# Performance work log

Hardware: AMD Instinct MI355X
Metric: run time of the kernel (lower is better)

Reference implementation:

```python
import jax, jax.numpy as jnp
import numpy as np

N, H, E, G, OUT = 50000, 128, 600000, 256, 64
NUM_ITERS = 5
GAMMA = 0.1
EPS = 0.1
NEG_SLOPE = 0.01


def setup_inputs() -> dict:
    key = jax.random.key(0)
    ks = jax.random.split(key, 10)
    s = 1.0 / np.sqrt(H)
    x = jax.random.normal(ks[0], (N, H), dtype=jnp.float32)
    edge_index = jax.random.randint(ks[1], (2, E), 0, N, dtype=jnp.int64)
    batch = jnp.sort(jax.random.randint(ks[2], (N,), 0, G, dtype=jnp.int64))
    W = jax.random.normal(ks[3], (H, H), dtype=jnp.float32) * s
    bias = jax.random.normal(ks[4], (H,), dtype=jnp.float32) * s
    lin_w = jax.random.normal(ks[5], (H, H), dtype=jnp.float32) * s
    l1_w = jax.random.normal(ks[6], (3 * H // 2, 3 * H), dtype=jnp.float32) / np.sqrt(3 * H)
    l1_b = jax.random.normal(ks[7], (3 * H // 2,), dtype=jnp.float32) * 0.01
    l2_w = jax.random.normal(ks[8], (OUT, 3 * H // 2), dtype=jnp.float32) / np.sqrt(3 * H // 2)
    l2_b = jax.random.normal(ks[9], (OUT,), dtype=jnp.float32) * 0.01
    return {"x": x, "edge_index": edge_index, "batch": batch, "W": W, "bias": bias,
            "lin_w": lin_w, "l1_w": l1_w, "l1_b": l1_b, "l2_w": l2_w, "l2_b": l2_b}


def reference(x, edge_index, batch, W, bias, lin_w, l1_w, l1_b, l2_w, l2_b):
    n = x.shape[0]
    src, dst = edge_index[0], edge_index[1]
    # antisymmetric weight: W - W^T - gamma*I
    A = W - W.T - GAMMA * jnp.eye(W.shape[0], dtype=x.dtype)
    for _ in range(NUM_ITERS):
        neigh = x @ lin_w.T                                   # [N,H] linear (no bias)
        agg = jax.ops.segment_sum(neigh[src], dst, num_segments=n)  # gather-scatter add
        conv = x @ A.T + agg + bias
        x = x + EPS * jnp.tanh(conv)
    # triple global pooling per graph: add / max / mean
    add = jax.ops.segment_sum(x, batch, num_segments=G)
    mx = jax.ops.segment_max(x, batch, num_segments=G)
    cnt = jax.ops.segment_sum(jnp.ones((n,), dtype=x.dtype), batch, num_segments=G)
    safe_cnt = jnp.maximum(cnt, 1.0)[:, None]
    mean = add / safe_cnt
    mx = jnp.where(cnt[:, None] > 0, mx, 0.0)
    pooled = jnp.concatenate([add, mx, mean], axis=1)          # [G, 3H]
    h = jax.nn.leaky_relu(pooled @ l1_w.T + l1_b, NEG_SLOPE)
    out = jax.nn.leaky_relu(h @ l2_w.T + l2_b, NEG_SLOPE)
    return out
```

## Files before the change

### kernel.cpp

```cpp
#include <hip/hip_runtime.h>
#include <hip/hip_fp16.h>
#include <cmath>

#define H 128
#define GAMMA 0.1f
#define EPS 0.1f
#define NEG 0.01f
#define NGRAPH 256

typedef _Float16 half_t;
typedef _Float16 f16x8 __attribute__((ext_vector_type(8)));
typedef _Float16 f16x4 __attribute__((ext_vector_type(4)));
typedef _Float16 f16x2 __attribute__((ext_vector_type(2)));
typedef float f32x4 __attribute__((ext_vector_type(4)));

__device__ __forceinline__ float fast_tanh(float v) {
    float e = __builtin_amdgcn_exp2f(v * 2.8853900817779268f);
    float r = __builtin_amdgcn_rcpf(e + 1.0f);
    return 1.0f - 2.0f * r;
}

__global__ void prep_kernel(const float* __restrict__ W, const float* __restrict__ lin_w,
                            half_t* __restrict__ WtT) {
    int idx = blockIdx.x * 256 + threadIdx.x;
    int j = idx >> 8, k = idx & 255;
    float v;
    if (k < H) v = W[j * H + k] - W[k * H + j] - (j == k ? GAMMA : 0.f);
    else       v = lin_w[j * H + (k - H)];
    WtT[j * 256 + k] = (half_t)v;
}

__global__ void cast_kernel(const float* __restrict__ x, half_t* __restrict__ xh, int n4) {
    int i = blockIdx.x * 256 + threadIdx.x;
    if (i < n4) {
        float4 v = *(const float4*)(x + (size_t)i * 4);
        half_t* o = xh + (size_t)i * 4;
        o[0] = (half_t)v.x; o[1] = (half_t)v.y; o[2] = (half_t)v.z; o[3] = (half_t)v.w;
    }
}

__global__ void count_kernel(const int* __restrict__ dst, int* __restrict__ deg, int E) {
    int e = blockIdx.x * blockDim.x + threadIdx.x;
    if (e < E) atomicAdd(&deg[dst[e]], 1);
}

#define SCHUNK 2048
__global__ __launch_bounds__(256) void scan_part(const int* __restrict__ deg,
                                                 int* __restrict__ partials, int N) {
    __shared__ int red[256];
    int t = threadIdx.x, b = blockIdx.x;
    int base = b * SCHUNK + t * 8;
    int s = 0;
#pragma unroll
    for (int i = 0; i < 8; ++i) { int idx = base + i; if (idx < N) s += deg[idx]; }
    red[t] = s;
    __syncthreads();
    for (int off = 128; off > 0; off >>= 1) {
        if (t < off) red[t] += red[t + off];
        __syncthreads();
    }
    if (t == 0) partials[b] = red[0];
}

__global__ void scan_mid(const int* __restrict__ partials, int* __restrict__ blkoff, int nblk) {
    int lane = threadIdx.x;
    int p = (lane < nblk) ? partials[lane] : 0;
    int v = p;
    for (int off = 1; off < 64; off <<= 1) {
        int u = __shfl_up(v, off);
        if (lane >= off) v += u;
    }
    if (lane < nblk) blkoff[lane] = v - p;
}

__global__ __launch_bounds__(256) void scan_final(const int* __restrict__ deg,
        const int* __restrict__ blkoff, int* __restrict__ row_start,
        int* __restrict__ cursor, int N, int E) {
    __shared__ int red[256];
    int t = threadIdx.x, b = blockIdx.x;
    int base = b * SCHUNK + t * 8;
    int v[8]; int s = 0;
#pragma unroll
    for (int i = 0; i < 8; ++i) { int idx = base + i; v[i] = (idx < N) ? deg[idx] : 0; s += v[i]; }
    red[t] = s;
    __syncthreads();
    for (int off = 1; off < 256; off <<= 1) {
        int u = (t >= off) ? red[t - off] : 0;
        __syncthreads();
        red[t] += u;
        __syncthreads();
    }
    int run = blkoff[b] + red[t] - s;
#pragma unroll
    for (int i = 0; i < 8; ++i) {
        int idx = base + i;
        if (idx < N) { row_start[idx] = run; cursor[idx] = run; run += v[i]; }
    }
    if (b == 0 && t == 0) row_start[N] = E;
}

__global__ void fill_kernel(const int* __restrict__ src, const int* __restrict__ dst,
                            int* __restrict__ cursor, int* __restrict__ csr_src, int E) {
    int e = blockIdx.x * blockDim.x + threadIdx.x;
    if (e < E) {
        int p = atomicAdd(&cursor[dst[e]], 1);
        csr_src[p] = src[e];
    }
}

__global__ __launch_bounds__(256) void gather_agg(const half_t* __restrict__ xh,
        const int* __restrict__ row_start, const int* __restrict__ csr_src,
        half_t* __restrict__ xaggh, int N) {
    int node = blockIdx.x * 4 + (threadIdx.x >> 6);
    if (node >= N) return;
    int lane = threadIdx.x & 63;
    int half = lane >> 5, li = lane & 31;
    int begin = row_start[node], end = row_start[node + 1];
    float a0 = 0.f, a1 = 0.f, a2 = 0.f, a3 = 0.f;
    float b0 = 0.f, b1 = 0.f, b2 = 0.f, b3 = 0.f;
    for (int base = begin; base < end; base += 64) {
        int cnt = min(64, end - base);
        int myidx = (lane < cnt) ? csr_src[base + lane] : 0;
        int j = 0;
        for (; j + 3 < cnt; j += 4) {
            int s0 = __shfl(myidx, j + half);
            int s1 = __shfl(myidx, j + 2 + half);
            f16x4 v0 = *(const f16x4*)(xh + (size_t)s0 * H + li * 4);
            f16x4 v1 = *(const f16x4*)(xh + (size_t)s1 * H + li * 4);
            a0 += (float)v0[0]; a1 += (float)v0[1]; a2 += (float)v0[2]; a3 += (float)v0[3];
            b0 += (float)v1[0]; b1 += (float)v1[1]; b2 += (float)v1[2]; b3 += (float)v1[3];
        }
        for (; j < cnt; j += 2) {
            if (j + half < cnt) {
                int s0 = __shfl(myidx, j + half);
                f16x4 v0 = *(const f16x4*)(xh + (size_t)s0 * H + li * 4);
                a0 += (float)v0[0]; a1 += (float)v0[1]; a2 += (float)v0[2]; a3 += (float)v0[3];
            }
        }
    }
    a0 += b0; a1 += b1; a2 += b2; a3 += b3;
    a0 += __shfl_xor(a0, 32); a1 += __shfl_xor(a1, 32);
    a2 += __shfl_xor(a2, 32); a3 += __shfl_xor(a3, 32);
    if (half == 0) {
        f16x4 o; o[0] = (half_t)a0; o[1] = (half_t)a1; o[2] = (half_t)a2; o[3] = (half_t)a3;
        *(f16x4*)(xaggh + (size_t)node * H + li * 4) = o;
    }
}

#define CROWS 128
#define BLDW 264
__global__ __launch_bounds__(256) void conv_mfma(
        const float* __restrict__ xin, const half_t* __restrict__ xh,
        const half_t* __restrict__ xaggh, const half_t* __restrict__ WtT,
        const float* __restrict__ bias,
        float* __restrict__ xout, half_t* __restrict__ xouth, int N) {
    __shared__ __align__(16) half_t sB[128 * BLDW];
    int tid = threadIdx.x;
    for (int c = tid; c < 4096; c += 256) {
        int j = c >> 5, off = (c & 31) * 8;
        *(f16x8*)&sB[j * BLDW + off] = *(const f16x8*)(WtT + j * 256 + off);
    }
    __syncthreads();

    int wave = tid >> 6, lane = tid & 63;
    int q = lane >> 4, m = lane & 15;
    int rowbase = blockIdx.x * CROWS + wave * 32;

    f32x4 acc[2][8];
#pragma unroll
    for (int rt = 0; rt < 2; ++rt)
#pragma unroll
        for (int ct = 0; ct < 8; ++ct) acc[rt][ct] = (f32x4){0.f, 0.f, 0.f, 0.f};

#pragma unroll
    for (int s = 0; s < 8; ++s) {
        const half_t* srcA = (s < 4) ? xh : xaggh;
        int koff = (s & 3) * 32 + q * 8;
        f16x8 afrag[2];
#pragma unroll
        for (int rt = 0; rt < 2; ++rt) {
            int row = rowbase + rt * 16 + m;
            row = min(row, N - 1);
            afrag[rt] = *(const f16x8*)(srcA + (size_t)row * H + koff);
        }
#pragma unroll
        for (int ct = 0; ct < 8; ++ct) {
            f16x8 bfrag = *(const f16x8*)&sB[(ct * 16 + m) * BLDW + s * 32 + q * 8];
            acc[0][ct] = __builtin_amdgcn_mfma_f32_16x16x32_f16(afrag[0], bfrag, acc[0][ct], 0, 0, 0);
            acc[1][ct] = __builtin_amdgcn_mfma_f32_16x16x32_f16(afrag[1], bfrag, acc[1][ct], 0, 0, 0);
        }
    }

#pragma unroll
    for (int rt = 0; rt < 2; ++rt) {
#pragma unroll
        for (int r = 0; r < 4; ++r) {
            int row = rowbase + rt * 16 + q * 4 + r;
            if (row < N) {
#pragma unroll
                for (int ct = 0; ct < 8; ++ct) {
                    int col = ct * 16 + m;
                    float c = acc[rt][ct][r] + bias[col];
                    float o = xin[(size_t)row * H + col] + EPS * fast_tanh(c);
                    xout[(size_t)row * H + col] = o;
                    xouth[(size_t)row * H + col] = (half_t)o;
                }
            }
        }
    }
}

__global__ __launch_bounds__(1024) void pool_kernel(const float* __restrict__ x,
        const int* __restrict__ batch, float* __restrict__ pooled, int N) {
    __shared__ float ssum[8][128];
    __shared__ float smax[8][128];
    int g = blockIdx.x, t = threadIdx.x;
    int feat = t & 127, slot = t >> 7;
    int lo = 0, hi = N;
    while (lo < hi) { int mid = (lo + hi) >> 1; if (batch[mid] < g) lo = mid + 1; else hi = mid; }
    int start = lo;
    hi = N;
    while (lo < hi) { int mid = (lo + hi) >> 1; if (batch[mid] < g + 1) lo = mid + 1; else hi = mid; }
    int end = lo;
    float sum = 0.f, mx = -INFINITY;
    for (int n = start + slot; n < end; n += 8) {
        float v = x[(size_t)n * H + feat];
        sum += v;
        mx = fmaxf(mx, v);
    }
    ssum[slot][feat] = sum;
    smax[slot][feat] = mx;
    __syncthreads();
    if (t < 128) {
        float s = 0.f, m = -INFINITY;
#pragma unroll
        for (int k = 0; k < 8; ++k) { s += ssum[k][t]; m = fmaxf(m, smax[k][t]); }
        int cnt = end - start;
        pooled[g * 384 + t] = s;
        pooled[g * 384 + 128 + t] = (cnt > 0) ? m : 0.f;
        pooled[g * 384 + 256 + t] = s / (float)(cnt > 0 ? cnt : 1);
    }
}

__global__ void mlp_kernel(const float* __restrict__ pooled, const float* __restrict__ l1_w,
                           const float* __restrict__ l1_b, const float* __restrict__ l2_w,
                           const float* __restrict__ l2_b, float* __restrict__ out) {
    __shared__ __align__(16) float sp[384];
    __shared__ __align__(16) float sh[192];
    int g = blockIdx.x, tid = threadIdx.x;
    for (int i = tid; i < 384; i += 256) sp[i] = pooled[g * 384 + i];
    __syncthreads();
    if (tid < 192) {
        float acc = l1_b[tid];
        const float* wr = l1_w + (size_t)tid * 384;
        for (int k = 0; k < 384; k += 4) {
            float4 w = *(const float4*)(wr + k);
            float4 p = *(const float4*)(sp + k);
            acc += w.x * p.x + w.y * p.y + w.z * p.z + w.w * p.w;
        }
        sh[tid] = acc > 0.f ? acc : NEG * acc;
    }
    __syncthreads();
    if (tid < 64) {
        float acc = l2_b[tid];
        const float* wr = l2_w + (size_t)tid * 192;
        for (int k = 0; k < 192; k += 4) {
            float4 w = *(const float4*)(wr + k);
            float4 p = *(const float4*)(sh + k);
            acc += w.x * p.x + w.y * p.y + w.z * p.z + w.w * p.w;
        }
        out[g * 64 + tid] = acc > 0.f ? acc : NEG * acc;
    }
}

extern "C" void kernel_launch(void* const* d_in, const int* in_sizes, int n_in,
                              void* d_out, int out_size, void* d_ws, size_t ws_size,
                              hipStream_t stream) {
    const float* x0    = (const float*)d_in[0];
    const int*   edge  = (const int*)d_in[1];
    const int*   batch = (const int*)d_in[2];
    const float* W     = (const float*)d_in[3];
    const float* bias  = (const float*)d_in[4];
    const float* lin_w = (const float*)d_in[5];
    const float* l1_w  = (const float*)d_in[6];
    const float* l1_b  = (const float*)d_in[7];
    const float* l2_w  = (const float*)d_in[8];
    const float* l2_b  = (const float*)d_in[9];
    float* out = (float*)d_out;

    int N = in_sizes[0] / H;
    int E = in_sizes[1] / 2;
    const int* src = edge;
    const int* dst = edge + E;

    size_t nh = (size_t)N * H;
    float* xA      = (float*)d_ws;
    float* xB      = xA + nh;
    float* pooled  = xB + nh;
    half_t* xhA    = (half_t*)(pooled + NGRAPH * 384);
    half_t* xhB    = xhA + nh;
    half_t* xaggh  = xhB + nh;
    half_t* WtT    = xaggh + nh;
    int* deg       = (int*)(WtT + 128 * 256);
    int* row_start = deg + N;
    int* cursor    = row_start + N + 1;
    int* csr_src   = cursor + N;
    int* partials  = csr_src + E;
    int* blkoff    = partials + 64;

    prep_kernel<<<128, 256, 0, stream>>>(W, lin_w, WtT);
    cast_kernel<<<((int)(nh / 4) + 255) / 256, 256, 0, stream>>>(x0, xhA, (int)(nh / 4));

    hipMemsetAsync(deg, 0, (size_t)N * sizeof(int), stream);
    count_kernel<<<(E + 255) / 256, 256, 0, stream>>>(dst, deg, E);
    int nblk = (N + SCHUNK - 1) / SCHUNK;
    scan_part<<<nblk, 256, 0, stream>>>(deg, partials, N);
    scan_mid<<<1, 64, 0, stream>>>(partials, blkoff, nblk);
    scan_final<<<nblk, 256, 0, stream>>>(deg, blkoff, row_start, cursor, N, E);
    fill_kernel<<<(E + 255) / 256, 256, 0, stream>>>(src, dst, cursor, csr_src, E);

    const float* xcur = x0;
    const half_t* xcur_h = xhA;
    for (int it = 0; it < 5; ++it) {
        gather_agg<<<(N + 3) / 4, 256, 0, stream>>>(xcur_h, row_start, csr_src, xaggh, N);
        float* xnext = (it & 1) ? xB : xA;
        half_t* xnext_h = (it & 1) ? xhA : xhB;
        conv_mfma<<<(N + CROWS - 1) / CROWS, 256, 0, stream>>>(
            xcur, xcur_h, xaggh, WtT, bias, xnext, xnext_h, N);
        xcur = xnext;
        xcur_h = xnext_h;
    }

    pool_kernel<<<NGRAPH, 1024, 0, stream>>>(xcur, batch, pooled, N);
    mlp_kernel<<<NGRAPH, 256, 0, stream>>>(pooled, l1_w, l1_b, l2_w, l2_b, out);
}
```

Before: 411.9 us.

## Fuse neighbor gather into MFMA conv kernel and merge pooling with MLP

Gathering and aggregation of neighbor features now happens inside the conv kernel. Each wave aggregates its 32 rows into shared memory, which removes the global xaggh write/read and one launch per iteration. The weight matrix is pre-permuted into MFMA fragment order so B fragments load straight from global/L2 instead of being staged in LDS. Other changes: the fp16 copy is skipped on the final iteration, and pool and MLP are fused into one kernel. Risk: the gather phase now runs with far fewer blocks (about 391 instead of 12500), which may reduce latency hiding and load balance for the irregular gather.

New measurement: 660.0 us. 60.3% more time.

```diff
diff --git a/kernel.cpp b/kernel.cpp
--- a/kernel.cpp
+++ b/kernel.cpp
@@ -11,7 +11,6 @@
 typedef _Float16 half_t;
 typedef _Float16 f16x8 __attribute__((ext_vector_type(8)));
 typedef _Float16 f16x4 __attribute__((ext_vector_type(4)));
-typedef _Float16 f16x2 __attribute__((ext_vector_type(2)));
 typedef float f32x4 __attribute__((ext_vector_type(4)));
 
 __device__ __forceinline__ float fast_tanh(float v) {
@@ -21,13 +20,19 @@
 }
 
 __global__ void prep_kernel(const float* __restrict__ W, const float* __restrict__ lin_w,
-                            half_t* __restrict__ WtT) {
+                            half_t* __restrict__ WtTf) {
     int idx = blockIdx.x * 256 + threadIdx.x;
-    int j = idx >> 8, k = idx & 255;
+    int t = idx & 7;
+    int lane = (idx >> 3) & 63;
+    int ct = (idx >> 9) & 7;
+    int s = idx >> 12;
+    int q = lane >> 4, m = lane & 15;
+    int j = ct * 16 + m;
+    int k = s * 32 + q * 8 + t;
     float v;
     if (k < H) v = W[j * H + k] - W[k * H + j] - (j == k ? GAMMA : 0.f);
     else       v = lin_w[j * H + (k - H)];
-    WtT[j * 256 + k] = (half_t)v;
+    WtTf[idx] = (half_t)v;
 }
 
 __global__ void cast_kernel(const float* __restrict__ x, half_t* __restrict__ xh, int n4) {
@@ -108,64 +113,72 @@
     }
 }
 
-__global__ __launch_bounds__(256) void gather_agg(const half_t* __restrict__ xh,
+#define CROWS 128
+#define AGLD 136
+__global__ __launch_bounds__(256) void fused_iter(
+        const float* __restrict__ xin, const half_t* __restrict__ xh,
         const int* __restrict__ row_start, const int* __restrict__ csr_src,
-        half_t* __restrict__ xaggh, int N) {
-    int node = blockIdx.x * 4 + (threadIdx.x >> 6);
-    if (node >= N) return;
-    int lane = threadIdx.x & 63;
+        const half_t* __restrict__ WtTf, const float* __restrict__ bias,
+        float* __restrict__ xout, half_t* __restrict__ xouth, int N, int write_h) {
+    __shared__ __align__(16) half_t sAgg[CROWS * AGLD];
+    int tid = threadIdx.x;
+    int wave = tid >> 6, lane = tid & 63;
     int half = lane >> 5, li = lane & 31;
-    int begin = row_start[node], end = row_start[node + 1];
-    float a0 = 0.f, a1 = 0.f, a2 = 0.f, a3 = 0.f;
-    float b0 = 0.f, b1 = 0.f, b2 = 0.f, b3 = 0.f;
-    for (int base = begin; base < end; base += 64) {
-        int cnt = min(64, end - base);
-        int myidx = (lane < cnt) ? csr_src[base + lane] : 0;
-        int j = 0;
-        for (; j + 3 < cnt; j += 4) {
-            int s0 = __shfl(myidx, j + half);
-            int s1 = __shfl(myidx, j + 2 + half);
-            f16x4 v0 = *(const f16x4*)(xh + (size_t)s0 * H + li * 4);
-            f16x4 v1 = *(const f16x4*)(xh + (size_t)s1 * H + li * 4);
-            a0 += (float)v0[0]; a1 += (float)v0[1]; a2 += (float)v0[2]; a3 += (float)v0[3];
-            b0 += (float)v1[0]; b1 += (float)v1[1]; b2 += (float)v1[2]; b3 += (float)v1[3];
-        }
-        for (; j < cnt; j += 2) {
-            if (j + half < cnt) {
+    int n0 = blockIdx.x * CROWS + wave * 32;
+
+    int ridx = n0 + (lane < 33 ? lane : 32);
+    ridx = min(ridx, N);
+    int rsl = row_start[ridx];
+
+    for (int i = 0; i < 32; ++i) {
+        int node = n0 + i;
+        if (node >= N) break;
+        int begin = __shfl(rsl, i);
+        int end   = __shfl(rsl, i + 1);
+        float a0 = 0.f, a1 = 0.f, a2 = 0.f, a3 = 0.f;
+        float b0 = 0.f, b1 = 0.f, b2 = 0.f, b3 = 0.f;
+        for (int base = begin; base < end; base += 64) {
+            int cnt = min(64, end - base);
+            int myidx = (lane < cnt) ? csr_src[base + lane] : 0;
+            int j = 0;
+            for (; j + 3 < cnt; j += 4) {
                 int s0 = __shfl(myidx, j + half);
+                int s1 = __shfl(myidx, j + 2 + half);
                 f16x4 v0 = *(const f16x4*)(xh + (size_t)s0 * H + li * 4);
+                f16x4 v1 = *(const f16x4*)(xh + (size_t)s1 * H + li * 4);
                 a0 += (float)v0[0]; a1 += (float)v0[1]; a2 += (float)v0[2]; a3 += (float)v0[3];
-            }
-        }
-    }
-    a0 += b0; a1 += b1; a2 += b2; a3 += b3;
-    a0 += __shfl_xor(a0, 32); a1 += __shfl_xor(a1, 32);
-    a2 += __shfl_xor(a2, 32); a3 += __shfl_xor(a3, 32);
-    if (half == 0) {
-        f16x4 o; o[0] = (half_t)a0; o[1] = (half_t)a1; o[2] = (half_t)a2; o[3] = (half_t)a3;
-        *(f16x4*)(xaggh + (size_t)node * H + li * 4) = o;
-    }
-}
-
-#define CROWS 128
-#define BLDW 264
-__global__ __launch_bounds__(256) void conv_mfma(
-        const float* __restrict__ xin, const half_t* __restrict__ xh,
-        const half_t* __restrict__ xaggh, const half_t* __restrict__ WtT,
-        const float* __restrict__ bias,
-        float* __restrict__ xout, half_t* __restrict__ xouth, int N) {
-    __shared__ __align__(16) half_t sB[128 * BLDW];
-    int tid = threadIdx.x;
-    for (int c = tid; c < 4096; c += 256) {
-        int j = c >> 5, off = (c & 31) * 8;
-        *(f16x8*)&sB[j * BLDW + off] = *(const f16x8*)(WtT + j * 256 + off);
-    }
-    __syncthreads();
-
-    int wave = tid >> 6, lane = tid & 63;
+                b0 += (float)v1[0]; b1 += (float)v1[1]; b2 += (float)v1[2]; b3 += (float)v1[3];
+            }
+            int rem = cnt - j;
+            if (rem > 0) {
+                int take = rem < 2 ? rem : 2;
+                int sel = j + (half < take ? half : 0);
+                int s0 = __shfl(myidx, sel);
+                f16x4 v0 = *(const f16x4*)(xh + (size_t)s0 * H + li * 4);
+                if (half < take) {
+                    a0 += (float)v0[0]; a1 += (float)v0[1]; a2 += (float)v0[2]; a3 += (float)v0[3];
+                }
+                j += take; rem -= take;
+            }
+            if (rem > 0) {
+                int s0 = __shfl(myidx, j);
+                f16x4 v0 = *(const f16x4*)(xh + (size_t)s0 * H + li * 4);
+                if (half == 0) {
+                    b0 += (float)v0[0]; b1 += (float)v0[1]; b2 += (float)v0[2]; b3 += (float)v0[3];
+                }
+            }
+        }
+        a0 += b0; a1 += b1; a2 += b2; a3 += b3;
+        a0 += __shfl_xor(a0, 32); a1 += __shfl_xor(a1, 32);
+        a2 += __shfl_xor(a2, 32); a3 += __shfl_xor(a3, 32);
+        if (half == 0) {
+            f16x4 o; o[0] = (half_t)a0; o[1] = (half_t)a1; o[2] = (half_t)a2; o[3] = (half_t)a3;
+            *(f16x4*)&sAgg[(wave * 32 + i) * AGLD + li * 4] = o;
+        }
+    }
+    __syncthreads();
+
     int q = lane >> 4, m = lane & 15;
-    int rowbase = blockIdx.x * CROWS + wave * 32;
-
     f32x4 acc[2][8];
 #pragma unroll
     for (int rt = 0; rt < 2; ++rt)
@@ -174,18 +187,20 @@
 
 #pragma unroll
     for (int s = 0; s < 8; ++s) {
-        const half_t* srcA = (s < 4) ? xh : xaggh;
-        int koff = (s & 3) * 32 + q * 8;
         f16x8 afrag[2];
 #pragma unroll
         for (int rt = 0; rt < 2; ++rt) {
-            int row = rowbase + rt * 16 + m;
-            row = min(row, N - 1);
-            afrag[rt] = *(const f16x8*)(srcA + (size_t)row * H + koff);
+            if (s < 4) {
+                int row = min(n0 + rt * 16 + m, N - 1);
+                afrag[rt] = *(const f16x8*)(xh + (size_t)row * H + s * 32 + q * 8);
+            } else {
+                afrag[rt] = *(const f16x8*)&sAgg[(wave * 32 + rt * 16 + m) * AGLD
+                                                 + (s - 4) * 32 + q * 8];
+            }
         }
 #pragma unroll
         for (int ct = 0; ct < 8; ++ct) {
-            f16x8 bfrag = *(const f16x8*)&sB[(ct * 16 + m) * BLDW + s * 32 + q * 8];
+            f16x8 bfrag = *(const f16x8*)(WtTf + ((s * 8 + ct) * 64 + lane) * 8);
             acc[0][ct] = __builtin_amdgcn_mfma_f32_16x16x32_f16(afrag[0], bfrag, acc[0][ct], 0, 0, 0);
             acc[1][ct] = __builtin_amdgcn_mfma_f32_16x16x32_f16(afrag[1], bfrag, acc[1][ct], 0, 0, 0);
         }
@@ -195,7 +210,7 @@
     for (int rt = 0; rt < 2; ++rt) {
 #pragma unroll
         for (int r = 0; r < 4; ++r) {
-            int row = rowbase + rt * 16 + q * 4 + r;
+            int row = n0 + rt * 16 + q * 4 + r;
             if (row < N) {
 #pragma unroll
                 for (int ct = 0; ct < 8; ++ct) {
@@ -203,17 +218,22 @@
                     float c = acc[rt][ct][r] + bias[col];
                     float o = xin[(size_t)row * H + col] + EPS * fast_tanh(c);
                     xout[(size_t)row * H + col] = o;
-                    xouth[(size_t)row * H + col] = (half_t)o;
+                    if (write_h) xouth[(size_t)row * H + col] = (half_t)o;
                 }
             }
         }
     }
 }
 
-__global__ __launch_bounds__(1024) void pool_kernel(const float* __restrict__ x,
-        const int* __restrict__ batch, float* __restrict__ pooled, int N) {
+__global__ __launch_bounds__(1024) void pool_mlp(const float* __restrict__ x,
+        const int* __restrict__ batch,
+        const float* __restrict__ l1_w, const float* __restrict__ l1_b,
+        const float* __restrict__ l2_w, const float* __restrict__ l2_b,
+        float* __restrict__ out, int N) {
     __shared__ float ssum[8][128];
     __shared__ float smax[8][128];
+    __shared__ __align__(16) float sp[384];
+    __shared__ __align__(16) float sh[192];
     int g = blockIdx.x, t = threadIdx.x;
     int feat = t & 127, slot = t >> 7;
     int lo = 0, hi = N;
@@ -236,40 +256,31 @@
 #pragma unroll
         for (int k = 0; k < 8; ++k) { s += ssum[k][t]; m = fmaxf(m, smax[k][t]); }
         int cnt = end - start;
-        pooled[g * 384 + t] = s;
-        pooled[g * 384 + 128 + t] = (cnt > 0) ? m : 0.f;
-        pooled[g * 384 + 256 + t] = s / (float)(cnt > 0 ? cnt : 1);
-    }
-}
-
-__global__ void mlp_kernel(const float* __restrict__ pooled, const float* __restrict__ l1_w,
-                           const float* __restrict__ l1_b, const float* __restrict__ l2_w,
-                           const float* __restrict__ l2_b, float* __restrict__ out) {
-    __shared__ __align__(16) float sp[384];
-    __shared__ __align__(16) float sh[192];
-    int g = blockIdx.x, tid = threadIdx.x;
-    for (int i = tid; i < 384; i += 256) sp[i] = pooled[g * 384 + i];
-    __syncthreads();
-    if (tid < 192) {
-        float acc = l1_b[tid];
-        const float* wr = l1_w + (size_t)tid * 384;
+        sp[t] = s;
+        sp[128 + t] = (cnt > 0) ? m : 0.f;
+        sp[256 + t] = s / (float)(cnt > 0 ? cnt : 1);
+    }
+    __syncthreads();
+    if (t < 192) {
+        float acc = l1_b[t];
+        const float* wr = l1_w + (size_t)t * 384;
         for (int k = 0; k < 384; k += 4) {
             float4 w = *(const float4*)(wr + k);
             float4 p = *(const float4*)(sp + k);
             acc += w.x * p.x + w.y * p.y + w.z * p.z + w.w * p.w;
         }
-        sh[tid] = acc > 0.f ? acc : NEG * acc;
-    }
-    __syncthreads();
-    if (tid < 64) {
-        float acc = l2_b[tid];
-        const float* wr = l2_w + (size_t)tid * 192;
+        sh[t] = acc > 0.f ? acc : NEG * acc;
+    }
+    __syncthreads();
+    if (t < 64) {
+        float acc = l2_b[t];
+        const float* wr = l2_w + (size_t)t * 192;
         for (int k = 0; k < 192; k += 4) {
             float4 w = *(const float4*)(wr + k);
             float4 p = *(const float4*)(sh + k);
             acc += w.x * p.x + w.y * p.y + w.z * p.z + w.w * p.w;
         }
-        out[g * 64 + tid] = acc > 0.f ? acc : NEG * acc;
+        out[g * 64 + t] = acc > 0.f ? acc : NEG * acc;
     }
 }
 
@@ -296,19 +307,17 @@
     size_t nh = (size_t)N * H;
     float* xA      = (float*)d_ws;
     float* xB      = xA + nh;
-    float* pooled  = xB + nh;
-    half_t* xhA    = (half_t*)(pooled + NGRAPH * 384);
+    half_t* xhA    = (half_t*)(xB + nh);
     half_t* xhB    = xhA + nh;
-    half_t* xaggh  = xhB + nh;
-    half_t* WtT    = xaggh + nh;
-    int* deg       = (int*)(WtT + 128 * 256);
+    half_t* WtTf   = xhB + nh;
+    int* deg       = (int*)(WtTf + 32768);
     int* row_start = deg + N;
     int* cursor    = row_start + N + 1;
     int* csr_src   = cursor + N;
     int* partials  = csr_src + E;
     int* blkoff    = partials + 64;
 
-    prep_kernel<<<128, 256, 0, stream>>>(W, lin_w, WtT);
+    prep_kernel<<<128, 256, 0, stream>>>(W, lin_w, WtTf);
     cast_kernel<<<((int)(nh / 4) + 255) / 256, 256, 0, stream>>>(x0, xhA, (int)(nh / 4));
 
     hipMemsetAsync(deg, 0, (size_t)N * sizeof(int), stream);
@@ -321,16 +330,15 @@
 
     const float* xcur = x0;
     const half_t* xcur_h = xhA;
+    int nblocks = (N + CROWS - 1) / CROWS;
     for (int it = 0; it < 5; ++it) {
-        gather_agg<<<(N + 3) / 4, 256, 0, stream>>>(xcur_h, row_start, csr_src, xaggh, N);
         float* xnext = (it & 1) ? xB : xA;
         half_t* xnext_h = (it & 1) ? xhA : xhB;
-        conv_mfma<<<(N + CROWS - 1) / CROWS, 256, 0, stream>>>(
-            xcur, xcur_h, xaggh, WtT, bias, xnext, xnext_h, N);
+        fused_iter<<<nblocks, 256, 0, stream>>>(
+            xcur, xcur_h, row_start, csr_src, WtTf, bias, xnext, xnext_h, N, it < 4 ? 1 : 0);
         xcur = xnext;
         xcur_h = xnext_h;
     }
 
-    pool_kernel<<<NGRAPH, 1024, 0, stream>>>(xcur, batch, pooled, N);
-    mlp_kernel<<<NGRAPH, 256, 0, stream>>>(pooled, l1_w, l1_b, l2_w, l2_b, out);
-}
+    pool_mlp<<<NGRAPH, 1024, 0, stream>>>(xcur, batch, l1_w, l1_b, l2_w, l2_b, out, N);
+}
```
